# Kernel tuning notes

Hardware: AMD Instinct MI355X
Metric: run time of the kernel (lower is better)

The kernel has to match this reference:

```python
import jax, jax.numpy as jnp
import numpy as np
import math

B, S, DIM, H = 2, 2048, 1024, 16
DH = DIM // H          # 64, per-head dim
DFF = 2048             # FCLayer hidden
NEG = -1.0e9


def setup_inputs() -> dict:
    key = jax.random.key(0)
    ks = jax.random.split(key, 10)
    glorot = jax.nn.initializers.glorot_uniform()
    de_x = jax.random.normal(ks[0], (B, S, DIM), dtype=jnp.float32)
    en_x = jax.random.normal(ks[1], (B, S, DIM), dtype=jnp.float32)
    # causal mask: 1.0 where attention is disallowed (upper triangle)
    mask = jnp.triu(jnp.ones((S, S), dtype=jnp.float32), k=1)
    # Stacked per-head projection weights for the (shared) attn_heads.
    Wq = glorot(ks[2], (H, DIM, DH), jnp.float32)
    Wk = glorot(ks[3], (H, DIM, DH), jnp.float32)
    Wv = glorot(ks[4], (H, DIM, DH), jnp.float32)
    W1 = glorot(ks[5], (DIM, DFF), jnp.float32)
    b1 = jnp.zeros((DFF,), jnp.float32)
    W2 = glorot(ks[6], (DFF, DIM), jnp.float32)
    b2 = jnp.zeros((DIM,), jnp.float32)
    return {"de_x": de_x, "en_x": en_x, "mask": mask,
            "Wq": Wq, "Wk": Wk, "Wv": Wv,
            "W1": W1, "b1": b1, "W2": W2, "b2": b2}


def _multihead(q_x, k_x, v_x, Wq, Wk, Wv, mask):
    # q_x/k_x/v_x: [B,S,DIM]; W*: [H,DIM,DH]
    q = jnp.einsum('bsd,hde->bhse', q_x, Wq)
    k = jnp.einsum('bsd,hde->bhse', k_x, Wk)
    v = jnp.einsum('bsd,hde->bhse', v_x, Wv)
    p = jnp.einsum('bhse,bhte->bhst', q, k) / math.sqrt(DH)
    if mask is not None:
        p = p + mask * NEG
    p = jax.nn.softmax(p, axis=-1)
    h = jnp.einsum('bhst,bhte->bhse', p, v)      # [B,H,S,DH]
    # concat heads along feature dim -> [B,S,DIM]
    return h.transpose(0, 2, 1, 3).reshape(q_x.shape[0], q_x.shape[1], -1)


def reference(de_x, en_x, mask, Wq, Wk, Wv, W1, b1, W2, b2):
    # Faithful to the source: compute_multihead_output ignores its attn_heads
    # arg and always uses self.attn_heads, and binds head(q=outer_en, k=outer_en,
    # v=outer_de). So:
    #   h1 = MHA(q=de_x, k=de_x, v=de_x, mask) with attn_heads weights
    #   h2 = MHA(q=en_x, k=en_x, v=h1, None)   with the SAME weights
    h1 = _multihead(de_x, de_x, de_x, Wq, Wk, Wv, mask)
    h2 = _multihead(en_x, en_x, h1, Wq, Wk, Wv, None)
    ff1 = jax.nn.relu(h2 @ W1 + b1)
    y = ff1 @ W2 + b2
    return y
```

## Files before the change

kernel.cpp:

```cpp
#include <hip/hip_runtime.h>
#include <stdint.h>


#define DEV static __device__ __forceinline__

typedef __attribute__((ext_vector_type(8))) __bf16 bf16x8;
typedef __attribute__((ext_vector_type(8))) unsigned short u16x8;
typedef __attribute__((ext_vector_type(4))) float f32x4;

DEV float bf2f(uint16_t u) { union { uint32_t u; float f; } v; v.u = ((uint32_t)u) << 16; return v.f; }
DEV uint16_t f2bf(float f) {
  union { float f; uint32_t u; } v; v.f = f;
  uint32_t r = v.u + 0x7fffu + ((v.u >> 16) & 1u);
  return (uint16_t)(r >> 16);
}
DEV uint16_t f2bf_hw(float f) { return __builtin_bit_cast(unsigned short, (__bf16)f); }

DEV bf16x8 asbf(u16x8 v) { return __builtin_bit_cast(bf16x8, v); }
DEV f32x4 mfma32(bf16x8 a, bf16x8 b, f32x4 c) {
  return __builtin_amdgcn_mfma_f32_16x16x32_bf16(a, b, c, 0, 0, 0);
}

DEV int swz(int row, int slot) { return slot ^ (row & 7); }

DEV bf16x8 frag8(const uint16_t* l, int row, int slot) {
  u16x8 v = *(const u16x8*)((const char*)l + row * 128 + (swz(row, slot) << 4));
  return asbf(v);
}

__global__ void probe_k(const uint32_t* __restrict__ mask, uint32_t* __restrict__ flag) {
  flag[0] = (mask[1] & 0xFFFFu) ? 1u : 0u;
}

__global__ __launch_bounds__(256) void cvt_k(const void* __restrict__ src,
                                             uint16_t* __restrict__ dst, int n,
                                             const uint32_t* __restrict__ flag) {
  const int isbf = (int)flag[0];
  const int stride = gridDim.x * 256 * 8;
  for (int i = (blockIdx.x * 256 + threadIdx.x) * 8; i < n; i += stride) {
    if (isbf) {
      *(u16x8*)(dst + i) = *(const u16x8*)((const uint16_t*)src + i);
    } else {
      const float* sf = (const float*)src + i;
      u16x8 o;
      for (int j = 0; j < 8; j++) o[j] = f2bf(sf[j]);
      *(u16x8*)(dst + i) = o;
    }
  }
}

__global__ __launch_bounds__(256) void transpose_k(const void* __restrict__ in_,
                                                   uint16_t* __restrict__ out, int R, int C,
                                                   float scale,
                                                   const uint32_t* __restrict__ flag) {
  __shared__ uint16_t t[32][33];
  const int isbf = (int)flag[0];
  const int b = blockIdx.z;
  const float* in_f = (const float*)in_ + (size_t)b * R * C;
  const uint16_t* in_u = (const uint16_t*)in_ + (size_t)b * R * C;
  out += (size_t)b * R * C;
  const int c0 = blockIdx.x * 32, r0 = blockIdx.y * 32;
  const int tx = threadIdx.x & 31, ty = threadIdx.x >> 5;
  for (int i = 0; i < 4; i++) {
    int r = ty + i * 8;
    size_t idx = (size_t)(r0 + r) * C + c0 + tx;
    uint16_t v;
    if (isbf) v = (scale == 1.0f) ? in_u[idx] : f2bf(bf2f(in_u[idx]) * scale);
    else      v = f2bf(in_f[idx] * scale);
    t[r][tx] = v;
  }
  __syncthreads();
  for (int i = 0; i < 4; i++) {
    int r = ty + i * 8;
    out[(size_t)(c0 + r) * R + r0 + tx] = t[tx][r];
  }
}

__global__ __launch_bounds__(256) void proj_k(
    const uint16_t* __restrict__ A_qk, const uint16_t* __restrict__ A_v,
    const uint16_t* __restrict__ Wt,
    uint16_t* __restrict__ Q, uint16_t* __restrict__ K, uint16_t* __restrict__ Vt) {
  __shared__ __attribute__((aligned(16))) uint16_t lA[2][128 * 64];
  __shared__ __attribute__((aligned(16))) uint16_t lB[2][128 * 64];
  const int tid = threadIdx.x, lane = tid & 63, wave = tid >> 6;
  const int g = lane >> 4;
  const int m0 = blockIdx.x * 128, n0 = blockIdx.y * 128;
  const int proj = n0 >> 10;
  const uint16_t* A = (proj == 2 ? A_v : A_qk);
  const uint16_t* Bt = Wt + (size_t)n0 * 1024;
  const int wm = wave >> 1, wn = wave & 1;
  f32x4 acc[4][4] = {};
  u16x8 ra[4], rb[4];
  const int row0 = tid >> 3, slot0 = tid & 7;
  auto loadT = [&](int kt) {
    for (int i = 0; i < 4; i++) {
      int row = row0 + i * 32;
      ra[i] = *(const u16x8*)(A + (size_t)(m0 + row) * 1024 + kt + slot0 * 8);
      rb[i] = *(const u16x8*)(Bt + (size_t)row * 1024 + kt + slot0 * 8);
    }
  };
  auto writeT = [&](int buf) {
    for (int i = 0; i < 4; i++) {
      int row = row0 + i * 32;
      *(u16x8*)&lA[buf][(row * 8 + swz(row, slot0)) * 8] = ra[i];
      *(u16x8*)&lB[buf][(row * 8 + swz(row, slot0)) * 8] = rb[i];
    }
  };
  loadT(0);
  writeT(0);
  int cur = 0;
  for (int it = 0; it < 16; it++) {
    const int more = (it < 15);
    if (more) loadT((it + 1) * 64);
    __syncthreads();
    for (int kk = 0; kk < 2; kk++) {
      bf16x8 af[4], bfr[4];
      for (int fm = 0; fm < 4; fm++) af[fm] = frag8(lA[cur], wm * 64 + fm * 16 + (lane & 15), kk * 4 + g);
      for (int fn = 0; fn < 4; fn++) bfr[fn] = frag8(lB[cur], wn * 64 + fn * 16 + (lane & 15), kk * 4 + g);
      for (int fm = 0; fm < 4; fm++)
        for (int fn = 0; fn < 4; fn++)
          acc[fm][fn] = mfma32(af[fm], bfr[fn], acc[fm][fn]);
    }
    if (more) writeT(cur ^ 1);
    cur ^= 1;
  }
  if (proj != 2) {
    uint16_t* outp = (proj == 0 ? Q : K);
    for (int fm = 0; fm < 4; fm++)
      for (int fn = 0; fn < 4; fn++)
        for (int r = 0; r < 4; r++) {
          int row = m0 + wm * 64 + fm * 16 + g * 4 + r;
          int b = row >> 11, s = row & 2047;
          int col = n0 + wn * 64 + fn * 16 + (lane & 15);
          int h = (col >> 6) & 15, e = col & 63;
          outp[(((size_t)(b * 16 + h)) * 2048 + s) * 64 + e] = f2bf(acc[fm][fn][r]);
        }
  } else {
    __syncthreads();
    uint16_t* tv = (uint16_t*)lA;
    for (int fm = 0; fm < 4; fm++)
      for (int fn = 0; fn < 4; fn++)
        for (int r = 0; r < 4; r++) {
          int rl = wm * 64 + fm * 16 + g * 4 + r;
          int cl = wn * 64 + fn * 16 + (lane & 15);
          int byte = rl * 2;
          *(uint16_t*)((char*)tv + cl * 256 + ((((byte >> 4)) ^ (cl & 15)) << 4) + (byte & 15)) =
              f2bf(acc[fm][fn][r]);
        }
    __syncthreads();
    const int b = m0 >> 11, s0 = m0 & 2047;
    const int c = tid >> 1, half = tid & 1;
    const int col = n0 + c;
    const int h = (col >> 6) & 15, e = col & 63;
    uint16_t* dst = Vt + (((size_t)(b * 16 + h)) * 64 + e) * 2048 + s0 + half * 64;
    for (int j = 0; j < 8; j++) {
      int rl = half * 64 + j * 8;
      u16x8 v = *(const u16x8*)((const char*)tv + c * 256 + (((rl >> 3) ^ (c & 15)) << 4));
      *(u16x8*)(dst + j * 8) = v;
    }
  }
}

template <int CAUSAL>
__global__ __launch_bounds__(256) void attn_k(const uint16_t* __restrict__ Q,
                                              const uint16_t* __restrict__ K,
                                              const uint16_t* __restrict__ Vt,
                                              uint16_t* __restrict__ Op0,
                                              uint16_t* __restrict__ Op1,
                                              float* __restrict__ lbuf) {
  __shared__ __attribute__((aligned(16))) uint16_t lK[64 * 64];
  __shared__ __attribute__((aligned(16))) uint16_t lV[64 * 64];
  __shared__ __attribute__((aligned(16))) uint16_t lP[4][16 * 64];
  const int tid = threadIdx.x, lane = tid & 63, wave = tid >> 6;
  const int g = lane >> 4;
  const int bx = blockIdx.x, h = blockIdx.y, b = blockIdx.z;
  int qt, split, kt0, kt1;
  if (CAUSAL) {
    if (bx < 32) {
      qt = 31 - (bx >> 1);
      split = bx & 1;
      int n0 = (qt + 1) >> 1;
      kt0 = split ? n0 : 0;
      kt1 = split ? (qt + 1) : n0;
    } else {
      qt = 47 - bx; split = 0; kt0 = 0; kt1 = qt + 1;
    }
  } else {
    qt = bx & 31; split = bx >> 5; kt0 = split * 16; kt1 = kt0 + 16;
  }
  const size_t bh = (size_t)(b * 16 + h);
  const uint16_t* Qg = Q + bh * 2048 * 64;
  const uint16_t* Kg = K + bh * 2048 * 64;
  const uint16_t* Vg = Vt + bh * 64 * 2048;
  uint16_t* lPw = lP[wave];
  bf16x8 ones;
  for (int j = 0; j < 8; j++) ones[j] = (__bf16)1.0f;
  uint32_t pbase[4];
  for (int r = 0; r < 4; r++) {
    int row = g * 4 + r;
    pbase[r] = row * 128 + (((((lane & 15) >> 3)) ^ (row & 7)) << 4) + ((lane & 7) << 1);
  }
  u16x8 rk[2], rv[2];
  const int row0 = tid >> 3, slot0 = tid & 7;
  auto loadKV = [&](int kt) {
    for (int i = 0; i < 2; i++) {
      int row = row0 + i * 32;
      rk[i] = *(const u16x8*)(Kg + (size_t)(kt * 64 + row) * 64 + slot0 * 8);
      rv[i] = *(const u16x8*)(Vg + (size_t)row * 2048 + kt * 64 + slot0 * 8);
    }
  };
  auto writeKV = [&]() {
    for (int i = 0; i < 2; i++) {
      int row = row0 + i * 32;
      *(u16x8*)&lK[(row * 8 + swz(row, slot0)) * 8] = rk[i];
      *(u16x8*)&lV[(row * 8 + swz(row, slot0)) * 8] = rv[i];
    }
  };
  const int q0 = qt * 64;
  bf16x8 qf[2];
  {
    int row = q0 + wave * 16 + (lane & 15);
    for (int kk = 0; kk < 2; kk++)
      qf[kk] = asbf(*(const u16x8*)(Qg + (size_t)row * 64 + kk * 32 + g * 8));
  }
  f32x4 oacc[4] = {};
  f32x4 acc_l = {};
  loadKV(kt0);
  for (int kt = kt0; kt < kt1; kt++) {
    const int more = (kt < kt1 - 1);
    __syncthreads();
    writeKV();
    __syncthreads();
    if (more) loadKV(kt + 1);
    f32x4 s[4] = {};
    for (int kk = 0; kk < 2; kk++)
      for (int nf = 0; nf < 4; nf++)
        s[nf] = mfma32(qf[kk], frag8(lK, nf * 16 + (lane & 15), kk * 4 + g), s[nf]);
    if (CAUSAL && kt == qt) {
      for (int nf = 0; nf < 4; nf++)
        for (int r = 0; r < 4; r++) {
          int qloc = wave * 16 + g * 4 + r;
          int kloc = nf * 16 + (lane & 15);
          if (kloc > qloc) s[nf][r] = -1e9f;
        }
    }
    for (int nf = 0; nf < 4; nf++)
      for (int r = 0; r < 4; r++) {
        float p = __builtin_amdgcn_exp2f(s[nf][r]);
        *(uint16_t*)((char*)lPw + (pbase[r] ^ (nf << 5))) = f2bf_hw(p);
      }
    for (int kk = 0; kk < 2; kk++) {
      bf16x8 pa = frag8(lPw, lane & 15, kk * 4 + g);
      acc_l = mfma32(pa, ones, acc_l);
      for (int df = 0; df < 4; df++)
        oacc[df] = mfma32(pa, frag8(lV, df * 16 + (lane & 15), kk * 4 + g), oacc[df]);
    }
  }
  uint16_t* Op = split ? Op1 : Op0;
  for (int df = 0; df < 4; df++)
    for (int r = 0; r < 4; r++) {
      int srow = q0 + wave * 16 + g * 4 + r;
      int e = df * 16 + (lane & 15);
      Op[((size_t)b * 2048 + srow) * 1024 + h * 64 + e] = f2bf(oacc[df][r]);
    }
  if ((lane & 15) == 0) {
    for (int r = 0; r < 4; r++) {
      int srow = q0 + wave * 16 + g * 4 + r;
      lbuf[((size_t)(split * 2 + b) * 16 + h) * 2048 + srow] = acc_l[r];
    }
  }
}

template <int CAUSAL>
__global__ __launch_bounds__(256) void merge_k(const uint16_t* __restrict__ O0,
                                               const uint16_t* __restrict__ O1,
                                               const float* __restrict__ lbuf,
                                               uint16_t* __restrict__ out) {
  int i = (blockIdx.x * 256 + threadIdx.x) * 8;
  int sg = i >> 10;
  int b = sg >> 11, s = sg & 2047;
  int h = (i & 1023) >> 6;
  size_t i0 = ((size_t)b * 16 + h) * 2048 + s;
  size_t i1 = ((size_t)(2 + b) * 16 + h) * 2048 + s;
  float l0 = lbuf[i0];
  u16x8 o0 = *(const u16x8*)(O0 + i);
  bool two = CAUSAL ? ((s >> 6) >= 16) : true;
  u16x8 o;
  if (two) {
    float inv = 1.f / (l0 + lbuf[i1]);
    u16x8 o1v = *(const u16x8*)(O1 + i);
    for (int j = 0; j < 8; j++)
      o[j] = f2bf((bf2f(o0[j]) + bf2f(o1v[j])) * inv);
  } else {
    float inv = 1.f / l0;
    for (int j = 0; j < 8; j++) o[j] = f2bf(bf2f(o0[j]) * inv);
  }
  *(u16x8*)(out + i) = o;
}

template <int RELU>
__global__ __launch_bounds__(256) void ff_k(const uint16_t* __restrict__ A,
                                            const uint16_t* __restrict__ Bt,
                                            const uint16_t* __restrict__ bias,
                                            uint16_t* __restrict__ C, int Kdim, int N) {
  __shared__ __attribute__((aligned(16))) uint16_t lA[2][128 * 64];
  __shared__ __attribute__((aligned(16))) uint16_t lB[2][128 * 64];
  const int tid = threadIdx.x, lane = tid & 63, wave = tid >> 6;
  const int g = lane >> 4;
  const int m0 = blockIdx.x * 128, n0 = blockIdx.y * 128;
  const int wm = wave >> 1, wn = wave & 1;
  f32x4 acc[4][4] = {};
  u16x8 ra[4], rb[4];
  const int row0 = tid >> 3, slot0 = tid & 7;
  auto loadT = [&](int kt) {
    for (int i = 0; i < 4; i++) {
      int row = row0 + i * 32;
      ra[i] = *(const u16x8*)(A + (size_t)(m0 + row) * Kdim + kt + slot0 * 8);
      rb[i] = *(const u16x8*)(Bt + (size_t)(n0 + row) * Kdim + kt + slot0 * 8);
    }
  };
  auto writeT = [&](int buf) {
    for (int i = 0; i < 4; i++) {
      int row = row0 + i * 32;
      *(u16x8*)&lA[buf][(row * 8 + swz(row, slot0)) * 8] = ra[i];
      *(u16x8*)&lB[buf][(row * 8 + swz(row, slot0)) * 8] = rb[i];
    }
  };
  loadT(0);
  writeT(0);
  int cur = 0;
  const int nit = Kdim >> 6;
  for (int it = 0; it < nit; it++) {
    const int more = (it < nit - 1);
    if (more) loadT((it + 1) * 64);
    __syncthreads();
    for (int kk = 0; kk < 2; kk++) {
      bf16x8 af[4], bfr[4];
      for (int fm = 0; fm < 4; fm++) af[fm] = frag8(lA[cur], wm * 64 + fm * 16 + (lane & 15), kk * 4 + g);
      for (int fn = 0; fn < 4; fn++) bfr[fn] = frag8(lB[cur], wn * 64 + fn * 16 + (lane & 15), kk * 4 + g);
      for (int fm = 0; fm < 4; fm++)
        for (int fn = 0; fn < 4; fn++)
          acc[fm][fn] = mfma32(af[fm], bfr[fn], acc[fm][fn]);
    }
    if (more) writeT(cur ^ 1);
    cur ^= 1;
  }
  for (int fm = 0; fm < 4; fm++)
    for (int fn = 0; fn < 4; fn++) {
      int col = n0 + wn * 64 + fn * 16 + (lane & 15);
      float bv = bf2f(bias[col]);
      for (int r = 0; r < 4; r++) {
        int row = m0 + wm * 64 + fm * 16 + g * 4 + r;
        float v = acc[fm][fn][r] + bv;
        if (RELU) v = fmaxf(v, 0.f);
        C[(size_t)row * N + col] = f2bf(v);
      }
    }
}

__global__ __launch_bounds__(256) void store_k(const uint16_t* __restrict__ yb,
                                               void* __restrict__ out, int n,
                                               const uint32_t* __restrict__ flag) {
  const int isbf = (int)flag[0];
  const int stride = gridDim.x * 256 * 8;
  for (int i = (blockIdx.x * 256 + threadIdx.x) * 8; i < n; i += stride) {
    u16x8 v = *(const u16x8*)(yb + i);
    if (isbf) {
      *(u16x8*)((uint16_t*)out + i) = v;
    } else {
      float* of = (float*)out + i;
      for (int j = 0; j < 8; j++) of[j] = bf2f(v[j]);
    }
  }
}

extern "C" void kernel_launch(void* const* d_in, const int* in_sizes, int n_in,
                              void* d_out, int out_size, void* d_ws, size_t ws_size,
                              hipStream_t stream) {
  const void* de_x = d_in[0];
  const void* en_x = d_in[1];
  const void* mask = d_in[2];
  const void* Wq = d_in[3];
  const void* Wk = d_in[4];
  const void* Wv = d_in[5];
  const void* W1 = d_in[6];
  const void* b1 = d_in[7];
  const void* W2 = d_in[8];
  const void* b2 = d_in[9];

  uint16_t* ws = (uint16_t*)d_ws;
  const size_t M1 = (size_t)1 << 20;
  uint32_t* flag = (uint32_t*)ws;
  uint16_t* b1c = ws + 1024;
  uint16_t* b2c = ws + 4096;
  float* lbuf = (float*)(ws + 8192);
  uint16_t* Wtq = ws + 1 * M1;
  uint16_t* Wtk = ws + 2 * M1;
  uint16_t* Wtv = ws + 3 * M1;
  uint16_t* W1t = ws + 4 * M1;
  uint16_t* W2t = ws + 6 * M1;
  uint16_t* de_c = ws + 8 * M1;
  uint16_t* en_c = ws + 12 * M1;
  uint16_t* Qb  = ws + 16 * M1;
  uint16_t* Kb  = ws + 20 * M1;
  uint16_t* Vtb = ws + 24 * M1;
  uint16_t* h1  = ws + 28 * M1;
  uint16_t* h2  = ws + 32 * M1;
  uint16_t* ff1 = Qb;
  uint16_t* yb  = Vtb;
  uint16_t* Op0 = de_c;
  uint16_t* Op1a = h2;
  uint16_t* Op1b = h1;

  const int NX = 2 * 2048 * 1024;
  dim3 blk(256);

  probe_k<<<1, 1, 0, stream>>>((const uint32_t*)mask, flag);
  cvt_k<<<2048, blk, 0, stream>>>(de_x, de_c, NX, flag);
  cvt_k<<<2048, blk, 0, stream>>>(en_x, en_c, NX, flag);
  cvt_k<<<1, blk, 0, stream>>>(b1, b1c, 2048, flag);
  cvt_k<<<1, blk, 0, stream>>>(b2, b2c, 1024, flag);
  transpose_k<<<dim3(2, 32, 16), blk, 0, stream>>>(Wq, Wtq, 1024, 64, 0.180336880f, flag);
  transpose_k<<<dim3(2, 32, 16), blk, 0, stream>>>(Wk, Wtk, 1024, 64, 1.0f, flag);
  transpose_k<<<dim3(2, 32, 16), blk, 0, stream>>>(Wv, Wtv, 1024, 64, 1.0f, flag);
  transpose_k<<<dim3(64, 32, 1), blk, 0, stream>>>(W1, W1t, 1024, 2048, 1.0f, flag);
  transpose_k<<<dim3(32, 64, 1), blk, 0, stream>>>(W2, W2t, 2048, 1024, 1.0f, flag);
  proj_k<<<dim3(32, 24), blk, 0, stream>>>(de_c, de_c, Wtq, Qb, Kb, Vtb);
  attn_k<1><<<dim3(48, 16, 2), blk, 0, stream>>>(Qb, Kb, Vtb, Op0, Op1a, lbuf);
  merge_k<1><<<2048, blk, 0, stream>>>(Op0, Op1a, lbuf, h1);
  proj_k<<<dim3(32, 24), blk, 0, stream>>>(en_c, h1, Wtq, Qb, Kb, Vtb);
  attn_k<0><<<dim3(64, 16, 2), blk, 0, stream>>>(Qb, Kb, Vtb, Op0, Op1b, lbuf);
  merge_k<0><<<2048, blk, 0, stream>>>(Op0, Op1b, lbuf, h2);
  ff_k<1><<<dim3(32, 16), blk, 0, stream>>>(h2, W1t, b1c, ff1, 1024, 2048);
  ff_k<0><<<dim3(32, 8), blk, 0, stream>>>(ff1, W2t, b2c, yb, 2048, 1024);
  store_k<<<2048, blk, 0, stream>>>(yb, d_out, out_size, flag);
}
```

Baseline: 276.8 us.

## Stage GEMM and attention tiles via direct global-to-LDS loads with double buffering

Replaces the register-staged global loads followed by LDS writes with buffer global_load_lds (direct-to-LDS) copies in the projection, FFN GEMM and attention kernels. Swizzling moves to the global-address side, and attention K/V gets double-buffered LDS so one barrier per tile suffices. The attention S computation is transposed (K as the A operand) so P can be written to LDS as packed 8-byte stores instead of scalar 16-bit stores. This frees registers and cuts LDS write instructions. The risk is correctness around async LDS-load completion: only __syncthreads is used, and no explicit vmcnt wait is visible.

After: 294.3 us. 6.4% more time.

```diff
diff --git a/kernel.cpp b/kernel.cpp
--- a/kernel.cpp
+++ b/kernel.cpp
@@ -6,6 +6,7 @@
 
 typedef __attribute__((ext_vector_type(8))) __bf16 bf16x8;
 typedef __attribute__((ext_vector_type(8))) unsigned short u16x8;
+typedef __attribute__((ext_vector_type(2))) uint32_t u32x2;
 typedef __attribute__((ext_vector_type(4))) float f32x4;
 
 DEV float bf2f(uint16_t u) { union { uint32_t u; float f; } v; v.u = ((uint32_t)u) << 16; return v.f; }
@@ -19,6 +20,12 @@
 DEV bf16x8 asbf(u16x8 v) { return __builtin_bit_cast(bf16x8, v); }
 DEV f32x4 mfma32(bf16x8 a, bf16x8 b, f32x4 c) {
   return __builtin_amdgcn_mfma_f32_16x16x32_bf16(a, b, c, 0, 0, 0);
+}
+
+DEV void gload_lds16(const void* g, void* l) {
+  __builtin_amdgcn_global_load_lds(
+      (const __attribute__((address_space(1))) uint32_t*)g,
+      (__attribute__((address_space(3))) uint32_t*)l, 16, 0, 0);
 }
 
 DEV int swz(int row, int slot) { return slot ^ (row & 7); }
@@ -90,29 +97,21 @@
   const uint16_t* Bt = Wt + (size_t)n0 * 1024;
   const int wm = wave >> 1, wn = wave & 1;
   f32x4 acc[4][4] = {};
-  u16x8 ra[4], rb[4];
-  const int row0 = tid >> 3, slot0 = tid & 7;
-  auto loadT = [&](int kt) {
+  const int lrow = lane >> 3, sl = lane & 7;
+  auto STAGE = [&](int buf, int kt) {
     for (int i = 0; i < 4; i++) {
-      int row = row0 + i * 32;
-      ra[i] = *(const u16x8*)(A + (size_t)(m0 + row) * 1024 + kt + slot0 * 8);
-      rb[i] = *(const u16x8*)(Bt + (size_t)row * 1024 + kt + slot0 * 8);
+      int cb = (i * 4 + wave) * 64;
+      int row = (cb >> 3) + lrow;
+      int so = swz(row, sl) << 3;
+      gload_lds16(A + (size_t)(m0 + row) * 1024 + kt + so, &lA[buf][cb * 8]);
+      gload_lds16(Bt + (size_t)row * 1024 + kt + so, &lB[buf][cb * 8]);
     }
   };
-  auto writeT = [&](int buf) {
-    for (int i = 0; i < 4; i++) {
-      int row = row0 + i * 32;
-      *(u16x8*)&lA[buf][(row * 8 + swz(row, slot0)) * 8] = ra[i];
-      *(u16x8*)&lB[buf][(row * 8 + swz(row, slot0)) * 8] = rb[i];
-    }
-  };
-  loadT(0);
-  writeT(0);
+  STAGE(0, 0);
   int cur = 0;
   for (int it = 0; it < 16; it++) {
-    const int more = (it < 15);
-    if (more) loadT((it + 1) * 64);
     __syncthreads();
+    if (it + 1 < 16) STAGE(cur ^ 1, (it + 1) * 64);
     for (int kk = 0; kk < 2; kk++) {
       bf16x8 af[4], bfr[4];
       for (int fm = 0; fm < 4; fm++) af[fm] = frag8(lA[cur], wm * 64 + fm * 16 + (lane & 15), kk * 4 + g);
@@ -121,7 +120,6 @@
         for (int fn = 0; fn < 4; fn++)
           acc[fm][fn] = mfma32(af[fm], bfr[fn], acc[fm][fn]);
     }
-    if (more) writeT(cur ^ 1);
     cur ^= 1;
   }
   if (proj != 2) {
@@ -137,7 +135,7 @@
         }
   } else {
     __syncthreads();
-    uint16_t* tv = (uint16_t*)lA;
+    uint16_t* tv = &lA[0][0];
     for (int fm = 0; fm < 4; fm++)
       for (int fn = 0; fn < 4; fn++)
         for (int r = 0; r < 4; r++) {
@@ -168,8 +166,8 @@
                                               uint16_t* __restrict__ Op0,
                                               uint16_t* __restrict__ Op1,
                                               float* __restrict__ lbuf) {
-  __shared__ __attribute__((aligned(16))) uint16_t lK[64 * 64];
-  __shared__ __attribute__((aligned(16))) uint16_t lV[64 * 64];
+  __shared__ __attribute__((aligned(16))) uint16_t lK[2][64 * 64];
+  __shared__ __attribute__((aligned(16))) uint16_t lV[2][64 * 64];
   __shared__ __attribute__((aligned(16))) uint16_t lP[4][16 * 64];
   const int tid = threadIdx.x, lane = tid & 63, wave = tid >> 6;
   const int g = lane >> 4;
@@ -195,25 +193,14 @@
   uint16_t* lPw = lP[wave];
   bf16x8 ones;
   for (int j = 0; j < 8; j++) ones[j] = (__bf16)1.0f;
-  uint32_t pbase[4];
-  for (int r = 0; r < 4; r++) {
-    int row = g * 4 + r;
-    pbase[r] = row * 128 + (((((lane & 15) >> 3)) ^ (row & 7)) << 4) + ((lane & 7) << 1);
-  }
-  u16x8 rk[2], rv[2];
-  const int row0 = tid >> 3, slot0 = tid & 7;
-  auto loadKV = [&](int kt) {
+  const int lrow = lane >> 3, sl = lane & 7;
+  auto STAGE = [&](int buf, int kt) {
     for (int i = 0; i < 2; i++) {
-      int row = row0 + i * 32;
-      rk[i] = *(const u16x8*)(Kg + (size_t)(kt * 64 + row) * 64 + slot0 * 8);
-      rv[i] = *(const u16x8*)(Vg + (size_t)row * 2048 + kt * 64 + slot0 * 8);
-    }
-  };
-  auto writeKV = [&]() {
-    for (int i = 0; i < 2; i++) {
-      int row = row0 + i * 32;
-      *(u16x8*)&lK[(row * 8 + swz(row, slot0)) * 8] = rk[i];
-      *(u16x8*)&lV[(row * 8 + swz(row, slot0)) * 8] = rv[i];
+      int cb = (i * 4 + wave) * 64;
+      int row = (cb >> 3) + lrow;
+      int so = swz(row, sl) << 3;
+      gload_lds16(Kg + (size_t)(kt * 64 + row) * 64 + so, &lK[buf][cb * 8]);
+      gload_lds16(Vg + (size_t)row * 2048 + kt * 64 + so, &lV[buf][cb * 8]);
     }
   };
   const int q0 = qt * 64;
@@ -225,36 +212,41 @@
   }
   f32x4 oacc[4] = {};
   f32x4 acc_l = {};
-  loadKV(kt0);
+  const int qrow = lane & 15;
+  STAGE(0, kt0);
+  int buf = 0;
   for (int kt = kt0; kt < kt1; kt++) {
-    const int more = (kt < kt1 - 1);
     __syncthreads();
-    writeKV();
-    __syncthreads();
-    if (more) loadKV(kt + 1);
+    if (kt + 1 < kt1) STAGE(buf ^ 1, kt + 1);
     f32x4 s[4] = {};
     for (int kk = 0; kk < 2; kk++)
       for (int nf = 0; nf < 4; nf++)
-        s[nf] = mfma32(qf[kk], frag8(lK, nf * 16 + (lane & 15), kk * 4 + g), s[nf]);
+        s[nf] = mfma32(frag8(lK[buf], nf * 16 + (lane & 15), kk * 4 + g), qf[kk], s[nf]);
     if (CAUSAL && kt == qt) {
       for (int nf = 0; nf < 4; nf++)
         for (int r = 0; r < 4; r++) {
-          int qloc = wave * 16 + g * 4 + r;
-          int kloc = nf * 16 + (lane & 15);
-          if (kloc > qloc) s[nf][r] = -1e9f;
+          int kloc = nf * 16 + g * 4 + r;
+          if (kloc > wave * 16 + qrow) s[nf][r] = -1e9f;
         }
     }
-    for (int nf = 0; nf < 4; nf++)
-      for (int r = 0; r < 4; r++) {
-        float p = __builtin_amdgcn_exp2f(s[nf][r]);
-        *(uint16_t*)((char*)lPw + (pbase[r] ^ (nf << 5))) = f2bf_hw(p);
-      }
+    for (int nf = 0; nf < 4; nf++) {
+      float p0 = __builtin_amdgcn_exp2f(s[nf][0]);
+      float p1 = __builtin_amdgcn_exp2f(s[nf][1]);
+      float p2 = __builtin_amdgcn_exp2f(s[nf][2]);
+      float p3 = __builtin_amdgcn_exp2f(s[nf][3]);
+      u32x2 w;
+      w[0] = ((uint32_t)f2bf_hw(p1) << 16) | f2bf_hw(p0);
+      w[1] = ((uint32_t)f2bf_hw(p3) << 16) | f2bf_hw(p2);
+      int slot = 2 * nf + (g >> 1);
+      *(u32x2*)((char*)lPw + qrow * 128 + ((slot ^ (qrow & 7)) << 4) + ((g & 1) << 3)) = w;
+    }
     for (int kk = 0; kk < 2; kk++) {
-      bf16x8 pa = frag8(lPw, lane & 15, kk * 4 + g);
+      bf16x8 pa = frag8(lPw, qrow, kk * 4 + g);
       acc_l = mfma32(pa, ones, acc_l);
       for (int df = 0; df < 4; df++)
-        oacc[df] = mfma32(pa, frag8(lV, df * 16 + (lane & 15), kk * 4 + g), oacc[df]);
-    }
+        oacc[df] = mfma32(pa, frag8(lV[buf], df * 16 + (lane & 15), kk * 4 + g), oacc[df]);
+    }
+    buf ^= 1;
   }
   uint16_t* Op = split ? Op1 : Op0;
   for (int df = 0; df < 4; df++)
@@ -310,30 +302,22 @@
   const int m0 = blockIdx.x * 128, n0 = blockIdx.y * 128;
   const int wm = wave >> 1, wn = wave & 1;
   f32x4 acc[4][4] = {};
-  u16x8 ra[4], rb[4];
-  const int row0 = tid >> 3, slot0 = tid & 7;
-  auto loadT = [&](int kt) {
+  const int lrow = lane >> 3, sl = lane & 7;
+  auto STAGE = [&](int buf, int kt) {
     for (int i = 0; i < 4; i++) {
-      int row = row0 + i * 32;
-      ra[i] = *(const u16x8*)(A + (size_t)(m0 + row) * Kdim + kt + slot0 * 8);
-      rb[i] = *(const u16x8*)(Bt + (size_t)(n0 + row) * Kdim + kt + slot0 * 8);
+      int cb = (i * 4 + wave) * 64;
+      int row = (cb >> 3) + lrow;
+      int so = swz(row, sl) << 3;
+      gload_lds16(A + (size_t)(m0 + row) * Kdim + kt + so, &lA[buf][cb * 8]);
+      gload_lds16(Bt + (size_t)(n0 + row) * Kdim + kt + so, &lB[buf][cb * 8]);
     }
   };
-  auto writeT = [&](int buf) {
-    for (int i = 0; i < 4; i++) {
-      int row = row0 + i * 32;
-      *(u16x8*)&lA[buf][(row * 8 + swz(row, slot0)) * 8] = ra[i];
-      *(u16x8*)&lB[buf][(row * 8 + swz(row, slot0)) * 8] = rb[i];
-    }
-  };
-  loadT(0);
-  writeT(0);
+  STAGE(0, 0);
   int cur = 0;
   const int nit = Kdim >> 6;
   for (int it = 0; it < nit; it++) {
-    const int more = (it < nit - 1);
-    if (more) loadT((it + 1) * 64);
     __syncthreads();
+    if (it + 1 < nit) STAGE(cur ^ 1, (it + 1) * 64);
     for (int kk = 0; kk < 2; kk++) {
       bf16x8 af[4], bfr[4];
       for (int fm = 0; fm < 4; fm++) af[fm] = frag8(lA[cur], wm * 64 + fm * 16 + (lane & 15), kk * 4 + g);
@@ -342,7 +326,6 @@
         for (int fn = 0; fn < 4; fn++)
           acc[fm][fn] = mfma32(af[fm], bfr[fn], acc[fm][fn]);
     }
-    if (more) writeT(cur ^ 1);
     cur ^= 1;
   }
   for (int fm = 0; fm < 4; fm++)
```

## Process two query tiles per attention block with direct global-to-LDS K/V loads

Applied to the files above, without the earlier changes.

Each attention block now handles a 128-row query pair instead of one 64-row tile, so every staged K/V tile feeds two sets of MFMAs and K/V traffic per query row halves. Staging uses global_load_lds straight into swizzled shared memory instead of going through registers, and P stores are packed into 64-bit writes. In exchange the grid halves, register pressure grows from the doubled accumulators, and the prefetch overlap of the old register double-buffer is lost because each tile is loaded then synced before compute.

Result: slower. 306.3 us (+10.7%).

```diff
diff --git a/kernel.cpp b/kernel.cpp
--- a/kernel.cpp
+++ b/kernel.cpp
@@ -6,6 +6,7 @@
 
 typedef __attribute__((ext_vector_type(8))) __bf16 bf16x8;
 typedef __attribute__((ext_vector_type(8))) unsigned short u16x8;
+typedef __attribute__((ext_vector_type(2))) uint32_t u32x2;
 typedef __attribute__((ext_vector_type(4))) float f32x4;
 
 DEV float bf2f(uint16_t u) { union { uint32_t u; float f; } v; v.u = ((uint32_t)u) << 16; return v.f; }
@@ -19,6 +20,12 @@
 DEV bf16x8 asbf(u16x8 v) { return __builtin_bit_cast(bf16x8, v); }
 DEV f32x4 mfma32(bf16x8 a, bf16x8 b, f32x4 c) {
   return __builtin_amdgcn_mfma_f32_16x16x32_bf16(a, b, c, 0, 0, 0);
+}
+
+DEV void gload_lds16(const void* g, void* l) {
+  __builtin_amdgcn_global_load_lds(
+      (const __attribute__((address_space(1))) uint32_t*)g,
+      (__attribute__((address_space(3))) uint32_t*)l, 16, 0, 0);
 }
 
 DEV int swz(int row, int slot) { return slot ^ (row & 7); }
@@ -170,104 +177,128 @@
                                               float* __restrict__ lbuf) {
   __shared__ __attribute__((aligned(16))) uint16_t lK[64 * 64];
   __shared__ __attribute__((aligned(16))) uint16_t lV[64 * 64];
-  __shared__ __attribute__((aligned(16))) uint16_t lP[4][16 * 64];
+  __shared__ __attribute__((aligned(16))) uint16_t lP[8][16 * 64];
   const int tid = threadIdx.x, lane = tid & 63, wave = tid >> 6;
-  const int g = lane >> 4;
+  const int g = lane >> 4, qrow = lane & 15;
   const int bx = blockIdx.x, h = blockIdx.y, b = blockIdx.z;
-  int qt, split, kt0, kt1;
+  int pair, split, kt0, kt1;
   if (CAUSAL) {
-    if (bx < 32) {
-      qt = 31 - (bx >> 1);
+    if (bx < 16) {
+      pair = 15 - (bx >> 1);
       split = bx & 1;
-      int n0 = (qt + 1) >> 1;
-      kt0 = split ? n0 : 0;
-      kt1 = split ? (qt + 1) : n0;
+      int half = pair + 1;
+      kt0 = split ? half : 0;
+      kt1 = split ? (2 * pair + 2) : half;
     } else {
-      qt = 47 - bx; split = 0; kt0 = 0; kt1 = qt + 1;
+      pair = 23 - bx; split = 0; kt0 = 0; kt1 = 2 * pair + 2;
     }
   } else {
-    qt = bx & 31; split = bx >> 5; kt0 = split * 16; kt1 = kt0 + 16;
-  }
+    pair = bx >> 1; split = bx & 1; kt0 = split * 16; kt1 = kt0 + 16;
+  }
+  const int q0 = pair * 128;
+  const int qtg0 = pair * 2, qtg1 = pair * 2 + 1;
   const size_t bh = (size_t)(b * 16 + h);
   const uint16_t* Qg = Q + bh * 2048 * 64;
   const uint16_t* Kg = K + bh * 2048 * 64;
   const uint16_t* Vg = Vt + bh * 64 * 2048;
-  uint16_t* lPw = lP[wave];
+  uint16_t* lP0 = lP[wave * 2];
+  uint16_t* lP1 = lP[wave * 2 + 1];
   bf16x8 ones;
   for (int j = 0; j < 8; j++) ones[j] = (__bf16)1.0f;
-  uint32_t pbase[4];
-  for (int r = 0; r < 4; r++) {
-    int row = g * 4 + r;
-    pbase[r] = row * 128 + (((((lane & 15) >> 3)) ^ (row & 7)) << 4) + ((lane & 7) << 1);
-  }
-  u16x8 rk[2], rv[2];
-  const int row0 = tid >> 3, slot0 = tid & 7;
-  auto loadKV = [&](int kt) {
+  const int lrow = lane >> 3, sl = lane & 7;
+  auto STAGE = [&](int kt) {
     for (int i = 0; i < 2; i++) {
-      int row = row0 + i * 32;
-      rk[i] = *(const u16x8*)(Kg + (size_t)(kt * 64 + row) * 64 + slot0 * 8);
-      rv[i] = *(const u16x8*)(Vg + (size_t)row * 2048 + kt * 64 + slot0 * 8);
-    }
-  };
-  auto writeKV = [&]() {
-    for (int i = 0; i < 2; i++) {
-      int row = row0 + i * 32;
-      *(u16x8*)&lK[(row * 8 + swz(row, slot0)) * 8] = rk[i];
-      *(u16x8*)&lV[(row * 8 + swz(row, slot0)) * 8] = rv[i];
-    }
-  };
-  const int q0 = qt * 64;
-  bf16x8 qf[2];
-  {
-    int row = q0 + wave * 16 + (lane & 15);
+      int cb = (i * 4 + wave) * 64;
+      int row = (cb >> 3) + lrow;
+      int so = swz(row, sl) << 3;
+      gload_lds16(Kg + (size_t)(kt * 64 + row) * 64 + so, &lK[cb * 8]);
+      gload_lds16(Vg + (size_t)row * 2048 + kt * 64 + so, &lV[cb * 8]);
+    }
+  };
+  bf16x8 qf[2][2];
+#pragma unroll
+  for (int grp = 0; grp < 2; grp++) {
+    int row = q0 + grp * 64 + wave * 16 + qrow;
     for (int kk = 0; kk < 2; kk++)
-      qf[kk] = asbf(*(const u16x8*)(Qg + (size_t)row * 64 + kk * 32 + g * 8));
-  }
-  f32x4 oacc[4] = {};
-  f32x4 acc_l = {};
-  loadKV(kt0);
+      qf[grp][kk] = asbf(*(const u16x8*)(Qg + (size_t)row * 64 + kk * 32 + g * 8));
+  }
+  f32x4 oacc[2][4] = {};
+  f32x4 acc_l[2] = {};
+  auto storeP = [&](uint16_t* lPw, f32x4 (&s)[4]) {
+#pragma unroll
+    for (int nf = 0; nf < 4; nf++) {
+      float p0 = __builtin_amdgcn_exp2f(s[nf][0]);
+      float p1 = __builtin_amdgcn_exp2f(s[nf][1]);
+      float p2 = __builtin_amdgcn_exp2f(s[nf][2]);
+      float p3 = __builtin_amdgcn_exp2f(s[nf][3]);
+      u32x2 w;
+      w[0] = ((uint32_t)f2bf_hw(p1) << 16) | f2bf_hw(p0);
+      w[1] = ((uint32_t)f2bf_hw(p3) << 16) | f2bf_hw(p2);
+      int slot = 2 * nf + (g >> 1);
+      *(u32x2*)((char*)lPw + qrow * 128 + ((slot ^ (qrow & 7)) << 4) + ((g & 1) << 3)) = w;
+    }
+  };
   for (int kt = kt0; kt < kt1; kt++) {
-    const int more = (kt < kt1 - 1);
-    __syncthreads();
-    writeKV();
-    __syncthreads();
-    if (more) loadKV(kt + 1);
-    f32x4 s[4] = {};
+    STAGE(kt);
+    __syncthreads();
+    const bool c0 = !CAUSAL || (kt <= qtg0);
+    f32x4 s0[4] = {}, s1[4] = {};
+#pragma unroll
     for (int kk = 0; kk < 2; kk++)
+#pragma unroll
+      for (int nf = 0; nf < 4; nf++) {
+        bf16x8 kf = frag8(lK, nf * 16 + qrow, kk * 4 + g);
+        if (c0) s0[nf] = mfma32(kf, qf[0][kk], s0[nf]);
+        s1[nf] = mfma32(kf, qf[1][kk], s1[nf]);
+      }
+    if (CAUSAL && kt == qtg0) {
+#pragma unroll
       for (int nf = 0; nf < 4; nf++)
-        s[nf] = mfma32(qf[kk], frag8(lK, nf * 16 + (lane & 15), kk * 4 + g), s[nf]);
-    if (CAUSAL && kt == qt) {
+        for (int r = 0; r < 4; r++)
+          if (nf * 16 + g * 4 + r > wave * 16 + qrow) s0[nf][r] = -1e9f;
+    }
+    if (CAUSAL && kt == qtg1) {
+#pragma unroll
       for (int nf = 0; nf < 4; nf++)
-        for (int r = 0; r < 4; r++) {
-          int qloc = wave * 16 + g * 4 + r;
-          int kloc = nf * 16 + (lane & 15);
-          if (kloc > qloc) s[nf][r] = -1e9f;
-        }
-    }
-    for (int nf = 0; nf < 4; nf++)
+        for (int r = 0; r < 4; r++)
+          if (nf * 16 + g * 4 + r > wave * 16 + qrow) s1[nf][r] = -1e9f;
+    }
+    if (c0) storeP(lP0, s0);
+    storeP(lP1, s1);
+#pragma unroll
+    for (int kk = 0; kk < 2; kk++) {
+      bf16x8 pa0, pa1;
+      if (c0) {
+        pa0 = frag8(lP0, qrow, kk * 4 + g);
+        acc_l[0] = mfma32(pa0, ones, acc_l[0]);
+      }
+      pa1 = frag8(lP1, qrow, kk * 4 + g);
+      acc_l[1] = mfma32(pa1, ones, acc_l[1]);
+#pragma unroll
+      for (int df = 0; df < 4; df++) {
+        bf16x8 vf = frag8(lV, df * 16 + qrow, kk * 4 + g);
+        if (c0) oacc[0][df] = mfma32(pa0, vf, oacc[0][df]);
+        oacc[1][df] = mfma32(pa1, vf, oacc[1][df]);
+      }
+    }
+    __syncthreads();
+  }
+  uint16_t* Op = split ? Op1 : Op0;
+#pragma unroll
+  for (int grp = 0; grp < 2; grp++)
+    for (int df = 0; df < 4; df++)
       for (int r = 0; r < 4; r++) {
-        float p = __builtin_amdgcn_exp2f(s[nf][r]);
-        *(uint16_t*)((char*)lPw + (pbase[r] ^ (nf << 5))) = f2bf_hw(p);
-      }
-    for (int kk = 0; kk < 2; kk++) {
-      bf16x8 pa = frag8(lPw, lane & 15, kk * 4 + g);
-      acc_l = mfma32(pa, ones, acc_l);
-      for (int df = 0; df < 4; df++)
-        oacc[df] = mfma32(pa, frag8(lV, df * 16 + (lane & 15), kk * 4 + g), oacc[df]);
-    }
-  }
-  uint16_t* Op = split ? Op1 : Op0;
-  for (int df = 0; df < 4; df++)
-    for (int r = 0; r < 4; r++) {
-      int srow = q0 + wave * 16 + g * 4 + r;
-      int e = df * 16 + (lane & 15);
-      Op[((size_t)b * 2048 + srow) * 1024 + h * 64 + e] = f2bf(oacc[df][r]);
-    }
-  if ((lane & 15) == 0) {
-    for (int r = 0; r < 4; r++) {
-      int srow = q0 + wave * 16 + g * 4 + r;
-      lbuf[((size_t)(split * 2 + b) * 16 + h) * 2048 + srow] = acc_l[r];
-    }
+        int srow = q0 + grp * 64 + wave * 16 + g * 4 + r;
+        int e = df * 16 + qrow;
+        Op[((size_t)b * 2048 + srow) * 1024 + h * 64 + e] = f2bf(oacc[grp][df][r]);
+      }
+  if (qrow == 0) {
+#pragma unroll
+    for (int grp = 0; grp < 2; grp++)
+      for (int r = 0; r < 4; r++) {
+        int srow = q0 + grp * 64 + wave * 16 + g * 4 + r;
+        lbuf[((size_t)(split * 2 + b) * 16 + h) * 2048 + srow] = acc_l[grp][r];
+      }
   }
 }
 
@@ -284,7 +315,7 @@
   size_t i1 = ((size_t)(2 + b) * 16 + h) * 2048 + s;
   float l0 = lbuf[i0];
   u16x8 o0 = *(const u16x8*)(O0 + i);
-  bool two = CAUSAL ? ((s >> 6) >= 16) : true;
+  bool two = CAUSAL ? (s >= 1024) : true;
   u16x8 o;
   if (two) {
     float inv = 1.f / (l0 + lbuf[i1]);
@@ -426,10 +457,10 @@
   transpose_k<<<dim3(64, 32, 1), blk, 0, stream>>>(W1, W1t, 1024, 2048, 1.0f, flag);
   transpose_k<<<dim3(32, 64, 1), blk, 0, stream>>>(W2, W2t, 2048, 1024, 1.0f, flag);
   proj_k<<<dim3(32, 24), blk, 0, stream>>>(de_c, de_c, Wtq, Qb, Kb, Vtb);
-  attn_k<1><<<dim3(48, 16, 2), blk, 0, stream>>>(Qb, Kb, Vtb, Op0, Op1a, lbuf);
+  attn_k<1><<<dim3(24, 16, 2), blk, 0, stream>>>(Qb, Kb, Vtb, Op0, Op1a, lbuf);
   merge_k<1><<<2048, blk, 0, stream>>>(Op0, Op1a, lbuf, h1);
   proj_k<<<dim3(32, 24), blk, 0, stream>>>(en_c, h1, Wtq, Qb, Kb, Vtb);
-  attn_k<0><<<dim3(64, 16, 2), blk, 0, stream>>>(Qb, Kb, Vtb, Op0, Op1b, lbuf);
+  attn_k<0><<<dim3(32, 16, 2), blk, 0, stream>>>(Qb, Kb, Vtb, Op0, Op1b, lbuf);
   merge_k<0><<<2048, blk, 0, stream>>>(Op0, Op1b, lbuf, h2);
   ff_k<1><<<dim3(32, 16), blk, 0, stream>>>(h2, W1t, b1c, ff1, 1024, 2048);
   ff_k<0><<<dim3(32, 8), blk, 0, stream>>>(ff1, W2t, b2c, yb, 2048, 1024);
```
